# Optimization experiments

Measured on AMD Instinct MI355X. Metric: run time of the kernel, lower is better.

The kernel has to match this reference:

```python
import jax, jax.numpy as jnp
import numpy as np

B, T, D = 8, 2048, 1024   # batch, seq_len (== block_size), n_embed
HS = 128                   # head_size

def setup_inputs() -> dict:
    key = jax.random.key(0)
    kx, kk, kq, kv = jax.random.split(key, 4)
    s = D ** -0.5  # torch Linear default init scale ~ U(-1/sqrt(in), 1/sqrt(in))
    x  = jax.random.normal(kx, (B, T, D), dtype=jnp.float32)
    Wk = jax.random.uniform(kk, (HS, D), jnp.float32, -s, s)
    Wq = jax.random.uniform(kq, (HS, D), jnp.float32, -s, s)
    Wv = jax.random.uniform(kv, (HS, D), jnp.float32, -s, s)
    return {"x": x, "Wk": Wk, "Wq": Wq, "Wv": Wv}

def reference(x, Wk, Wq, Wv):
    # single-head causal self-attention; dropout disabled (eval mode)
    Tlen = x.shape[1]
    k = jnp.einsum('btd,hd->bth', x, Wk)   # [B,T,HS]
    q = jnp.einsum('btd,hd->bth', x, Wq)
    v = jnp.einsum('btd,hd->bth', x, Wv)
    scale = Wk.shape[0] ** -0.5
    scores = jnp.einsum('bth,bsh->bts', q, k) * scale   # [B,T,T]
    causal = jnp.tril(jnp.ones((Tlen, Tlen), dtype=bool))
    scores = jnp.where(causal, scores, -jnp.inf)
    weights = jax.nn.softmax(scores, axis=-1)
    out = jnp.einsum('bts,bsh->bth', weights, v)        # [B,T,HS]
    return out
```

## Files before the change

kernel.cpp:

```cpp
#include <hip/hip_runtime.h>
#include <hip/hip_bf16.h>
#include <math.h>

#define BATCH_N 8
#define SEQ_T   2048
#define DIM_D   1024
#define HS_N    128

using bf16x8_t = __attribute__((ext_vector_type(8))) __bf16;
using bf16x4_t = __attribute__((ext_vector_type(4))) __bf16;
using f32x4_t  = __attribute__((ext_vector_type(4))) float;

__device__ __forceinline__ f32x4_t mfma_16x16x32(bf16x8_t a, bf16x8_t b, f32x4_t c) {
  return __builtin_amdgcn_mfma_f32_16x16x32_bf16(a, b, c, 0, 0, 0);
}

__device__ __forceinline__ void async_cp16(const void* g, void* l) {
  __builtin_amdgcn_global_load_lds(
      (const __attribute__((address_space(1))) unsigned int*)g,
      (__attribute__((address_space(3))) unsigned int*)l, 16, 0, 0);
}

#define BAR()      __builtin_amdgcn_s_barrier()
#define FENCE()    asm volatile("" ::: "memory")
#define WAIT_VM(n) asm volatile("s_waitcnt vmcnt(" #n ")" ::: "memory")
#define WAIT_LGKM0 asm volatile("s_waitcnt lgkmcnt(0)" ::: "memory")

__global__ __launch_bounds__(256) void castw_kernel(
    const float* __restrict__ Wk, const float* __restrict__ Wq,
    const float* __restrict__ Wv, __bf16* __restrict__ Wb,
    unsigned int* __restrict__ km) {
  if (blockIdx.x == 0 && threadIdx.x < 8) km[threadIdx.x] = 0u;
  int idx = blockIdx.x * 256 + threadIdx.x;
  int e   = idx * 4;
  int row = e >> 10;
  int col = e & 1023;
  const float* src;
  float sc = 1.0f;
  if (row < 128) {
    src = Wk + row * DIM_D + col;
  } else if (row < 256) {
    src = Wq + (row - 128) * DIM_D + col;
    sc  = 0.08838834764831845f;
  } else {
    src = Wv + (row - 256) * DIM_D + col;
  }
  float4 v = *(const float4*)src;
  bf16x4_t o;
  o[0] = (__bf16)(v.x * sc); o[1] = (__bf16)(v.y * sc);
  o[2] = (__bf16)(v.z * sc); o[3] = (__bf16)(v.w * sc);
  *(bf16x4_t*)(Wb + e) = o;
}

__global__ __launch_bounds__(512, 1) void proj_kernel(
    const float* __restrict__ x, const __bf16* __restrict__ Wb,
    __bf16* __restrict__ Qb, __bf16* __restrict__ Kb, __bf16* __restrict__ Vt,
    unsigned int* __restrict__ km) {
  __shared__ __align__(16) char psmem[131072];
  __bf16* A = (__bf16*)psmem;

  const int tid  = threadIdx.x;
  const int lane = tid & 63;
  const int wave = tid >> 6;
  const int h    = wave >> 2;
  const int g    = wave & 3;
  const int lr = lane & 15;
  const int lq = lane >> 4;
  const int m0 = blockIdx.x * 64;

  f32x4_t acc[2][6];
  #pragma unroll
  for (int mt = 0; mt < 2; ++mt)
    #pragma unroll
    for (int nt = 0; nt < 6; ++nt) acc[mt][nt] = (f32x4_t){0.f, 0.f, 0.f, 0.f};

  auto stageB = [&](int kt) {
    __bf16* Bs = (__bf16*)(psmem + 32768 + (kt & 3) * 24576);
    for (int c = wave; c < 24; c += 8) {
      const int row = c * 16 + (lane >> 2);
      const int u   = (lane & 3) ^ ((row >> 1) & 3);
      async_cp16(Wb + (size_t)row * DIM_D + kt * 32 + u * 8, Bs + c * 512);
    }
  };

  stageB(0);
  stageB(1);

  for (int p = 0; p < 4; ++p) {
    __syncthreads();

    {
      const int r  = tid >> 3;
      const int t  = tid & 7;
      const float* xs = x + (size_t)(m0 + r) * DIM_D + p * 256;
      __bf16* as = A + r * 256;
      const int sw = r & 7;
      #pragma unroll
      for (int i = 0; i < 4; ++i) {
        const int u = t + 8 * i;
        float4 f0 = *(const float4*)(xs + u * 8);
        float4 f1 = *(const float4*)(xs + u * 8 + 4);
        bf16x8_t a;
        a[0] = (__bf16)f0.x; a[1] = (__bf16)f0.y;
        a[2] = (__bf16)f0.z; a[3] = (__bf16)f0.w;
        a[4] = (__bf16)f1.x; a[5] = (__bf16)f1.y;
        a[6] = (__bf16)f1.z; a[7] = (__bf16)f1.w;
        *(bf16x8_t*)(as + ((u ^ sw) * 8)) = a;
      }
    }
    __syncthreads();

    for (int kt2 = 0; kt2 < 8; ++kt2) {
      const int kt = p * 8 + kt2;
      if (kt + 2 < 32) {
        stageB(kt + 2);
        WAIT_VM(6);
      } else if (kt == 30) {
        WAIT_VM(3);
      } else {
        WAIT_VM(0);
      }
      BAR();
      FENCE();
      const __bf16* Bs = (const __bf16*)(psmem + 32768 + (kt & 3) * 24576);

      bf16x8_t af[2];
      #pragma unroll
      for (int mt = 0; mt < 2; ++mt) {
        const int ml = h * 32 + mt * 16 + lr;
        const int u  = kt2 * 4 + lq;
        af[mt] = *(const bf16x8_t*)(&A[ml * 256 + ((u ^ (ml & 7)) * 8)]);
      }
      bf16x8_t bfv[6];
      #pragma unroll
      for (int nt = 0; nt < 6; ++nt) {
        const int nl = g * 96 + nt * 16 + lr;
        bfv[nt] = *(const bf16x8_t*)(&Bs[nl * 32 + ((lq ^ ((nl >> 1) & 3)) * 8)]);
      }
      #pragma unroll
      for (int mt = 0; mt < 2; ++mt)
        #pragma unroll
        for (int nt = 0; nt < 6; ++nt)
          acc[mt][nt] = mfma_16x16x32(af[mt], bfv[nt], acc[mt][nt]);
    }
  }

  __syncthreads();
  float* rowss = (float*)psmem;
  if (tid < 64) rowss[tid] = 0.f;
  __syncthreads();
  if (g < 2) {
    #pragma unroll
    for (int mt = 0; mt < 2; ++mt)
      #pragma unroll
      for (int r = 0; r < 4; ++r) {
        float s = 0.f;
        #pragma unroll
        for (int nt = 0; nt < 6; ++nt)
          if (g == 0 || nt < 2) s += acc[mt][nt][r] * acc[mt][nt][r];
        s += __shfl_xor(s, 1); s += __shfl_xor(s, 2);
        s += __shfl_xor(s, 4); s += __shfl_xor(s, 8);
        if (lr == 0) atomicAdd(&rowss[h * 32 + mt * 16 + lq * 4 + r], s);
      }
  }
  __syncthreads();
  if (tid < 64) {
    float v = rowss[tid];
    #pragma unroll
    for (int off = 1; off < 64; off <<= 1) v = fmaxf(v, __shfl_xor(v, off));
    if (tid == 0) atomicMax(km + (m0 >> 11), __float_as_uint(v));
  }

  #pragma unroll
  for (int mt = 0; mt < 2; ++mt) {
    const int t0 = m0 + h * 32 + mt * 16 + lq * 4;
    #pragma unroll
    for (int nt = 0; nt < 6; ++nt) {
      const int nn = g * 96 + nt * 16 + lr;
      if (nn < 256) {
        __bf16* dst = (nn < 128) ? (Kb + nn) : (Qb + (nn - 128));
        #pragma unroll
        for (int r = 0; r < 4; ++r)
          dst[(size_t)(t0 + r) * HS_N] = (__bf16)acc[mt][nt][r];
      } else {
        const int bb = t0 >> 11;
        const int tl = t0 & 2047;
        bf16x4_t o;
        #pragma unroll
        for (int r = 0; r < 4; ++r) o[r] = (__bf16)acc[mt][nt][r];
        *(bf16x4_t*)(Vt + (size_t)bb * (HS_N * SEQ_T) + (size_t)(nn - 256) * SEQ_T + tl) = o;
      }
    }
  }
}

__global__ __launch_bounds__(256, 2) void attn_kernel(
    const __bf16* __restrict__ Qb, const __bf16* __restrict__ Kb,
    const __bf16* __restrict__ Vt, const unsigned int* __restrict__ km,
    __bf16* __restrict__ Opart, float* __restrict__ lpart) {
  __shared__ __align__(16) char smem[81920];
  __bf16* KsBase = (__bf16*)smem;
  __bf16* VsBase = (__bf16*)(smem + 32768);
  float*  Ofl    = (float*)smem;

  const int lane = threadIdx.x & 63;
  const int wave = threadIdx.x >> 6;
  const int lr = lane & 15;
  const int lq = lane >> 4;
  const int bid  = blockIdx.x;
  const int b    = bid & 7;
  const int rest = bid >> 3;
  const int jg   = 15 - (rest >> 2);
  const int p4   = rest & 3;
  const int Q0   = jg * 128;
  const int qa   = Q0 + wave * 32;
  const int ch   = 2 * (jg + 1);
  const int c0   = (p4 * ch) >> 2;
  const int c1   = ((p4 + 1) * ch) >> 2;

  const __bf16* Qbb = Qb + (size_t)b * (SEQ_T * HS_N);
  const __bf16* Kbb = Kb + (size_t)b * (SEQ_T * HS_N);
  const __bf16* Vbb = Vt + (size_t)b * (HS_N * SEQ_T);
  __bf16* pbA = (__bf16*)(smem + 65536 + wave * 4096);
  __bf16* pbB = (__bf16*)(smem + 65536 + wave * 4096 + 2048);

  bf16x8_t qf[2][4];
  #pragma unroll
  for (int t = 0; t < 2; ++t)
    #pragma unroll
    for (int ks = 0; ks < 4; ++ks)
      qf[t][ks] = *(const bf16x8_t*)(Qbb + (size_t)(qa + t * 16 + lr) * HS_N
                                     + ks * 32 + lq * 8);

  const float km2 = __uint_as_float(km[b]);
  float mrow[2][4];
  #pragma unroll
  for (int t = 0; t < 2; ++t) {
    float qn2 = 0.f;
    #pragma unroll
    for (int ks = 0; ks < 4; ++ks)
      #pragma unroll
      for (int j = 0; j < 8; ++j) { float f = (float)qf[t][ks][j]; qn2 += f * f; }
    qn2 += __shfl_xor(qn2, 16);
    qn2 += __shfl_xor(qn2, 32);
    #pragma unroll
    for (int r2 = 0; r2 < 4; ++r2)
      mrow[t][r2] = sqrtf(__shfl(qn2, lq * 4 + r2) * km2);
  }

  f32x4_t Oa[2][8];
  #pragma unroll
  for (int t = 0; t < 2; ++t)
    #pragma unroll
    for (int o = 0; o < 8; ++o) Oa[t][o] = (f32x4_t){0.f, 0.f, 0.f, 0.f};
  float lsum[2][4] = {{0.f,0.f,0.f,0.f},{0.f,0.f,0.f,0.f}};

  auto stage = [&](int bufi, int c) {
    const int kk = c * 64;
    __bf16* Ks = KsBase + bufi * 8192;
    for (int idx = wave; idx < 32; idx += 4) {
      if (idx < 16) {
        const int row = idx * 4 + (lane >> 4);
        const int u   = (lane & 15) ^ (row & 15);
        async_cp16(Kbb + (size_t)(kk + row) * HS_N + u * 8, Ks + idx * 512);
      } else {
        const int i2  = idx - 16;
        const int row = i2 * 8 + (lane >> 3);
        const int u   = (lane & 7) ^ (row & 7);
        async_cp16(Vbb + (size_t)row * SEQ_T + kk + u * 8, VsBase + bufi * 8192 + i2 * 512);
      }
    }
  };

  if (c0 < c1) stage(0, c0);
  __syncthreads();

  for (int c = c0; c < c1; ++c) {
    const int cur = (c - c0) & 1;
    if (c + 1 < c1) {
      stage(cur ^ 1, c + 1);
      WAIT_VM(8);
    } else {
      WAIT_VM(0);
    }
    BAR();
    FENCE();

    const int kk = c * 64;
    const __bf16* Ks = KsBase + cur * 8192;
    const __bf16* Vs = VsBase + cur * 8192;

    f32x4_t s0[4], s1[4];
    #pragma unroll
    for (int nt = 0; nt < 4; ++nt) {
      s0[nt] = (f32x4_t){0.f, 0.f, 0.f, 0.f};
      s1[nt] = (f32x4_t){0.f, 0.f, 0.f, 0.f};
    }
    #pragma unroll
    for (int ks = 0; ks < 4; ++ks)
      #pragma unroll
      for (int nt = 0; nt < 4; ++nt) {
        bf16x8_t kf = *(const bf16x8_t*)(
            &Ks[(nt * 16 + lr) * 128 + (((ks * 4 + lq) ^ lr) * 8)]);
        s0[nt] = mfma_16x16x32(qf[0][ks], kf, s0[nt]);
        s1[nt] = mfma_16x16x32(qf[1][ks], kf, s1[nt]);
      }
    const int q0a = qa, q0b = qa + 16;
    if (kk + 63 > q0a) {
      #pragma unroll
      for (int nt = 0; nt < 4; ++nt) {
        const int col = kk + nt * 16 + lr;
        #pragma unroll
        for (int r2 = 0; r2 < 4; ++r2)
          if (col > q0a + lq * 4 + r2) s0[nt][r2] = -INFINITY;
      }
    }
    if (kk + 63 > q0b) {
      #pragma unroll
      for (int nt = 0; nt < 4; ++nt) {
        const int col = kk + nt * 16 + lr;
        #pragma unroll
        for (int r2 = 0; r2 < 4; ++r2)
          if (col > q0b + lq * 4 + r2) s1[nt][r2] = -INFINITY;
      }
    }

    #pragma unroll
    for (int r2 = 0; r2 < 4; ++r2) {
      float a0 = __expf(s0[0][r2] - mrow[0][r2]);
      float a1 = __expf(s0[1][r2] - mrow[0][r2]);
      float a2 = __expf(s0[2][r2] - mrow[0][r2]);
      float a3 = __expf(s0[3][r2] - mrow[0][r2]);
      s0[0][r2] = a0; s0[1][r2] = a1; s0[2][r2] = a2; s0[3][r2] = a3;
      lsum[0][r2] += (a0 + a1) + (a2 + a3);
      float b0 = __expf(s1[0][r2] - mrow[1][r2]);
      float b1 = __expf(s1[1][r2] - mrow[1][r2]);
      float b2 = __expf(s1[2][r2] - mrow[1][r2]);
      float b3 = __expf(s1[3][r2] - mrow[1][r2]);
      s1[0][r2] = b0; s1[1][r2] = b1; s1[2][r2] = b2; s1[3][r2] = b3;
      lsum[1][r2] += (b0 + b1) + (b2 + b3);
    }

    #pragma unroll
    for (int nt = 0; nt < 4; ++nt)
      #pragma unroll
      for (int r2 = 0; r2 < 4; ++r2) {
        const int prow = lq * 4 + r2;
        const int pcol = (nt * 16 + lr) ^ ((prow & 7) << 3);
        pbA[prow * 64 + pcol] = (__bf16)s0[nt][r2];
        pbB[prow * 64 + pcol] = (__bf16)s1[nt][r2];
      }

    #pragma unroll
    for (int k2 = 0; k2 < 2; ++k2) {
      const int au = ((k2 * 4 + lq) ^ (lr & 7)) << 3;
      bf16x8_t afrA = *(const bf16x8_t*)(pbA + lr * 64 + au);
      bf16x8_t afrB = *(const bf16x8_t*)(pbB + lr * 64 + au);
      #pragma unroll
      for (int o = 0; o < 8; ++o) {
        bf16x8_t vfr = *(const bf16x8_t*)(
            &Vs[(o * 16 + lr) * 64 + (((k2 * 4 + lq) ^ (lr & 7)) * 8)]);
        Oa[0][o] = mfma_16x16x32(afrA, vfr, Oa[0][o]);
        Oa[1][o] = mfma_16x16x32(afrB, vfr, Oa[1][o]);
      }
    }
    WAIT_LGKM0;
    BAR();
    FENCE();
  }

  #pragma unroll
  for (int t = 0; t < 2; ++t)
    #pragma unroll
    for (int r2 = 0; r2 < 4; ++r2) {
      float v = lsum[t][r2];
      v += __shfl_xor(v, 1);
      v += __shfl_xor(v, 2);
      v += __shfl_xor(v, 4);
      v += __shfl_xor(v, 8);
      if (lr == 0)
        lpart[bid * 128 + wave * 32 + t * 16 + lq * 4 + r2] = v;
    }

  #pragma unroll
  for (int t = 0; t < 2; ++t)
    #pragma unroll
    for (int o = 0; o < 8; ++o)
      #pragma unroll
      for (int r2 = 0; r2 < 4; ++r2)
        Ofl[(wave * 32 + t * 16 + lq * 4 + r2) * 132 + o * 16 + lr] = Oa[t][o][r2];
  __syncthreads();

  {
    const int row = threadIdx.x >> 1;
    const int cb  = (threadIdx.x & 1) * 64;
    __bf16* dst = Opart + ((size_t)bid * 128 + row) * 128 + cb;
    #pragma unroll
    for (int g2 = 0; g2 < 16; ++g2) {
      float4 f = *(const float4*)(&Ofl[row * 132 + cb + g2 * 4]);
      bf16x4_t o;
      o[0] = (__bf16)f.x; o[1] = (__bf16)f.y; o[2] = (__bf16)f.z; o[3] = (__bf16)f.w;
      *(bf16x4_t*)(dst + g2 * 4) = o;
    }
  }
}

__global__ __launch_bounds__(256) void merge_kernel(
    const __bf16* __restrict__ Opart, const float* __restrict__ lpart,
    float* __restrict__ out) {
  const int idx = blockIdx.x * 256 + threadIdx.x;
  const int row = idx >> 5;
  const int c4  = (idx & 31) * 4;
  const int b   = row >> 11;
  const int tl  = row & 2047;
  const int jg  = tl >> 7;
  const int lrow = tl & 127;
  const int rbase = (15 - jg) * 4;
  float a0 = 0.f, a1 = 0.f, a2 = 0.f, a3 = 0.f, l = 0.f;
  #pragma unroll
  for (int p = 0; p < 4; ++p) {
    const int s = b + 8 * (rbase + p);
    bf16x4_t a = *(const bf16x4_t*)(Opart + ((size_t)s * 128 + lrow) * 128 + c4);
    a0 += (float)a[0]; a1 += (float)a[1]; a2 += (float)a[2]; a3 += (float)a[3];
    l += lpart[s * 128 + lrow];
  }
  const float inv = 1.0f / l;
  float4 o;
  o.x = a0 * inv; o.y = a1 * inv; o.z = a2 * inv; o.w = a3 * inv;
  *(float4*)(out + (size_t)row * HS_N + c4) = o;
}

extern "C" void kernel_launch(void* const* d_in, const int* in_sizes, int n_in,
                              void* d_out, int out_size, void* d_ws, size_t ws_size,
                              hipStream_t stream) {
  const float* x  = (const float*)d_in[0];
  const float* Wk = (const float*)d_in[1];
  const float* Wq = (const float*)d_in[2];
  const float* Wv = (const float*)d_in[3];
  float* out = (float*)d_out;

  char* ws = (char*)d_ws;
  __bf16* Wb = (__bf16*)ws;
  __bf16* Qb = (__bf16*)(ws + 786432);
  __bf16* Kb = (__bf16*)(ws + 786432 + 4194304);
  __bf16* Vt = (__bf16*)(ws + 786432 + 8388608);
  unsigned int* km = (unsigned int*)(ws + 13369344);
  __bf16* Opart = (__bf16*)(ws + 13369600);
  float*  lpart = (float*)(ws + 30146816);

  castw_kernel<<<384, 256, 0, stream>>>(Wk, Wq, Wv, Wb, km);
  proj_kernel<<<256, 512, 0, stream>>>(x, Wb, Qb, Kb, Vt, km);
  attn_kernel<<<512, 256, 0, stream>>>(Qb, Kb, Vt, km, Opart, lpart);
  merge_kernel<<<2048, 256, 0, stream>>>(Opart, lpart, out);
}
```

Baseline: 148.3 us.

## Pipeline x cast in projection and balance causal attention splits per query block

The projection kernel now double-buffers the fp32-to-bf16 cast of x in 128-column chunks. Global loads for the next chunk are issued via inline asm while the current chunk's MFMAs run, which removes the two full-block syncs per phase. The attention split-K partitioning changes from a fixed 4 splits per query block to a variable count chosen by lookup tables, scaled to the causal work. This drops the grid from 512 to 488 blocks and aims to even out per-block work. The merge kernel reads the matching variable number of partials, at the cost of a non-unrolled loop and table lookups.

Measured after the change: 145.6 us. Within noise of the previous version (-1.8%).

```diff
diff --git a/kernel.cpp b/kernel.cpp
--- a/kernel.cpp
+++ b/kernel.cpp
@@ -25,6 +25,14 @@
 #define FENCE()    asm volatile("" ::: "memory")
 #define WAIT_VM(n) asm volatile("s_waitcnt vmcnt(" #n ")" ::: "memory")
 #define WAIT_LGKM0 asm volatile("s_waitcnt lgkmcnt(0)" ::: "memory")
+#define SCHEDBAR() __builtin_amdgcn_sched_barrier(0)
+
+__device__ const unsigned char SJG[61] = {
+  15,15,15,15,15,15,15, 14,14,14,14,14,14, 13,13,13,13,13,13,
+  12,12,12,12,12,12, 11,11,11,11,11, 10,10,10,10,10,
+  9,9,9,9, 8,8,8,8, 7,7,7,7, 6,6,6, 5,5,5, 4,4, 3,3, 2,2, 1, 0};
+__device__ const unsigned char PT[16] = {1,1,2,2,2,3,3,4,4,4,5,5,6,6,6,7};
+__device__ const unsigned char BS[16] = {60,59,57,55,53,50,47,43,39,35,30,25,19,13,7,0};
 
 __global__ __launch_bounds__(256) void castw_kernel(
     const float* __restrict__ Wk, const float* __restrict__ Wq,
@@ -57,7 +65,6 @@
     __bf16* __restrict__ Qb, __bf16* __restrict__ Kb, __bf16* __restrict__ Vt,
     unsigned int* __restrict__ km) {
   __shared__ __align__(16) char psmem[131072];
-  __bf16* A = (__bf16*)psmem;
 
   const int tid  = threadIdx.x;
   const int lane = tid & 63;
@@ -83,45 +90,61 @@
     }
   };
 
+  const int cr = tid >> 3;
+  const int cu = tid & 7;
+  f32x4_t xr0, xr1, xr2, xr3;
+  auto castLoad = [&](int sp) {
+    const float* xs = x + (size_t)(m0 + cr) * DIM_D + sp * 128;
+    const float* p0 = xs + cu * 8;
+    const float* p1 = xs + cu * 8 + 4;
+    const float* p2 = xs + (cu + 8) * 8;
+    const float* p3 = xs + (cu + 8) * 8 + 4;
+    asm volatile("global_load_dwordx4 %0, %1, off" : "=&v"(xr0) : "v"(p0));
+    asm volatile("global_load_dwordx4 %0, %1, off" : "=&v"(xr1) : "v"(p1));
+    asm volatile("global_load_dwordx4 %0, %1, off" : "=&v"(xr2) : "v"(p2));
+    asm volatile("global_load_dwordx4 %0, %1, off" : "=&v"(xr3) : "v"(p3));
+  };
+  auto castStore = [&](int sp) {
+    __bf16* as = (__bf16*)(psmem + (sp & 1) * 16384) + cr * 128;
+    const int sw = cr & 7;
+    bf16x8_t a0, a1;
+    a0[0] = (__bf16)xr0[0]; a0[1] = (__bf16)xr0[1];
+    a0[2] = (__bf16)xr0[2]; a0[3] = (__bf16)xr0[3];
+    a0[4] = (__bf16)xr1[0]; a0[5] = (__bf16)xr1[1];
+    a0[6] = (__bf16)xr1[2]; a0[7] = (__bf16)xr1[3];
+    a1[0] = (__bf16)xr2[0]; a1[1] = (__bf16)xr2[1];
+    a1[2] = (__bf16)xr2[2]; a1[3] = (__bf16)xr2[3];
+    a1[4] = (__bf16)xr3[0]; a1[5] = (__bf16)xr3[1];
+    a1[6] = (__bf16)xr3[2]; a1[7] = (__bf16)xr3[3];
+    *(bf16x8_t*)(as + ((cu ^ sw) * 8))       = a0;
+    *(bf16x8_t*)(as + (((cu + 8) ^ sw) * 8)) = a1;
+  };
+
+  castLoad(0);
   stageB(0);
   stageB(1);
-
-  for (int p = 0; p < 4; ++p) {
-    __syncthreads();
-
-    {
-      const int r  = tid >> 3;
-      const int t  = tid & 7;
-      const float* xs = x + (size_t)(m0 + r) * DIM_D + p * 256;
-      __bf16* as = A + r * 256;
-      const int sw = r & 7;
-      #pragma unroll
-      for (int i = 0; i < 4; ++i) {
-        const int u = t + 8 * i;
-        float4 f0 = *(const float4*)(xs + u * 8);
-        float4 f1 = *(const float4*)(xs + u * 8 + 4);
-        bf16x8_t a;
-        a[0] = (__bf16)f0.x; a[1] = (__bf16)f0.y;
-        a[2] = (__bf16)f0.z; a[3] = (__bf16)f0.w;
-        a[4] = (__bf16)f1.x; a[5] = (__bf16)f1.y;
-        a[6] = (__bf16)f1.z; a[7] = (__bf16)f1.w;
-        *(bf16x8_t*)(as + ((u ^ sw) * 8)) = a;
-      }
-    }
-    __syncthreads();
-
-    for (int kt2 = 0; kt2 < 8; ++kt2) {
-      const int kt = p * 8 + kt2;
-      if (kt + 2 < 32) {
-        stageB(kt + 2);
-        WAIT_VM(6);
-      } else if (kt == 30) {
-        WAIT_VM(3);
+  WAIT_VM(6);
+  SCHEDBAR();
+  castStore(0);
+  WAIT_LGKM0;
+  BAR(); FENCE();
+
+  for (int p = 0; p < 8; ++p) {
+    #pragma unroll
+    for (int kt2 = 0; kt2 < 4; ++kt2) {
+      const int kt = p * 4 + kt2;
+      if (kt + 2 < 32) stageB(kt + 2);
+      if (p < 7) {
+        if (kt2 == 0 || kt2 == 3) { WAIT_VM(6); } else { WAIT_VM(10); }
       } else {
-        WAIT_VM(0);
-      }
-      BAR();
-      FENCE();
+        if (kt2 == 0 || kt2 == 1)      { WAIT_VM(6); }
+        else if (kt2 == 2)             { WAIT_VM(3); }
+        else                           { WAIT_VM(0); }
+      }
+      BAR(); FENCE();
+      if (p < 7 && kt2 == 0) castLoad(p + 1);
+
+      const __bf16* As = (const __bf16*)(psmem + (p & 1) * 16384);
       const __bf16* Bs = (const __bf16*)(psmem + 32768 + (kt & 3) * 24576);
 
       bf16x8_t af[2];
@@ -129,7 +152,7 @@
       for (int mt = 0; mt < 2; ++mt) {
         const int ml = h * 32 + mt * 16 + lr;
         const int u  = kt2 * 4 + lq;
-        af[mt] = *(const bf16x8_t*)(&A[ml * 256 + ((u ^ (ml & 7)) * 8)]);
+        af[mt] = *(const bf16x8_t*)(&As[ml * 128 + ((u ^ (ml & 7)) * 8)]);
       }
       bf16x8_t bfv[6];
       #pragma unroll
@@ -142,7 +165,16 @@
         #pragma unroll
         for (int nt = 0; nt < 6; ++nt)
           acc[mt][nt] = mfma_16x16x32(af[mt], bfv[nt], acc[mt][nt]);
-    }
+
+      if (p < 7 && kt2 == 2) {
+        SCHEDBAR();
+        WAIT_VM(6);
+        SCHEDBAR();
+        castStore(p + 1);
+      }
+    }
+    WAIT_LGKM0;
+    BAR(); FENCE();
   }
 
   __syncthreads();
@@ -209,14 +241,15 @@
   const int lq = lane >> 4;
   const int bid  = blockIdx.x;
   const int b    = bid & 7;
-  const int rest = bid >> 3;
-  const int jg   = 15 - (rest >> 2);
-  const int p4   = rest & 3;
+  const int slot = bid >> 3;
+  const int jg   = SJG[slot];
+  const int pp   = slot - BS[jg];
+  const int P    = PT[jg];
   const int Q0   = jg * 128;
   const int qa   = Q0 + wave * 32;
   const int ch   = 2 * (jg + 1);
-  const int c0   = (p4 * ch) >> 2;
-  const int c1   = ((p4 + 1) * ch) >> 2;
+  const int c0   = (pp * ch) / P;
+  const int c1   = ((pp + 1) * ch) / P;
 
   const __bf16* Qbb = Qb + (size_t)b * (SEQ_T * HS_N);
   const __bf16* Kbb = Kb + (size_t)b * (SEQ_T * HS_N);
@@ -415,11 +448,11 @@
   const int tl  = row & 2047;
   const int jg  = tl >> 7;
   const int lrow = tl & 127;
-  const int rbase = (15 - jg) * 4;
+  const int P    = PT[jg];
+  const int base = BS[jg];
   float a0 = 0.f, a1 = 0.f, a2 = 0.f, a3 = 0.f, l = 0.f;
-  #pragma unroll
-  for (int p = 0; p < 4; ++p) {
-    const int s = b + 8 * (rbase + p);
+  for (int p = 0; p < P; ++p) {
+    const int s = b + 8 * (base + p);
     bf16x4_t a = *(const bf16x4_t*)(Opart + ((size_t)s * 128 + lrow) * 128 + c4);
     a0 += (float)a[0]; a1 += (float)a[1]; a2 += (float)a[2]; a3 += (float)a[3];
     l += lpart[s * 128 + lrow];
@@ -450,6 +483,6 @@
 
   castw_kernel<<<384, 256, 0, stream>>>(Wk, Wq, Wv, Wb, km);
   proj_kernel<<<256, 512, 0, stream>>>(x, Wb, Qb, Kb, Vt, km);
-  attn_kernel<<<512, 256, 0, stream>>>(Qb, Kb, Vt, km, Opart, lpart);
+  attn_kernel<<<488, 256, 0, stream>>>(Qb, Kb, Vt, km, Opart, lpart);
   merge_kernel<<<2048, 256, 0, stream>>>(Opart, lpart, out);
 }
```
